# Optimization experiments

Measured on AMD Instinct MI355X. Metric: run time of the kernel, lower is better.

## Reference

```python
import jax, jax.numpy as jnp
import numpy as np

N_ITER = 3
N_CLASS = 10
N_ROUTE = 1152  # 32*6*6

def _conv(x, w, b, stride):
    y = jax.lax.conv_general_dilated(x, w, window_strides=(stride, stride), padding='VALID',
                                     dimension_numbers=('NCHW', 'OIHW', 'NCHW'))
    return y + b[None, :, None, None]

def setup_inputs() -> dict:
    key = jax.random.key(0)
    ks = jax.random.split(key, 7)
    B = 256
    return {
        'x': jax.random.normal(ks[0], (B, 1, 28, 28), jnp.float32),
        'conv1_w': jax.random.normal(ks[1], (256, 1, 9, 9), jnp.float32) * 0.05,
        'conv1_b': jax.random.normal(ks[2], (256,), jnp.float32) * 0.05,
        'conv2_w': jax.random.normal(ks[3], (256, 256, 9, 9), jnp.float32) * 0.02,
        'conv2_b': jax.random.normal(ks[4], (256,), jnp.float32) * 0.02,
        'W': jax.random.normal(ks[5], (10, 32, 6, 6, 16, 8), jnp.float32) * 0.1,
        'Wb': jax.random.normal(ks[6], (10, 32, 6, 6, 16), jnp.float32) * 0.1,
    }

def reference(x, conv1_w, conv1_b, conv2_w, conv2_b, W, Wb):
    # conv1 (no activation, matching the original forward)
    h = _conv(x, conv1_w, conv1_b, 1)                 # [B,256,20,20]
    prim = _conv(h, conv2_w, conv2_b, 2)              # [B,256,6,6]
    prim = prim.reshape(-1, 32, 6, 6, 8)              # same raw .view as torch
    # fused per-location linear: u_hat[b,j,k,l,i,o]
    u_hat = jnp.einsum('bjklc,ijkloc->bjklio', prim, W) + Wb.transpose(1, 2, 3, 0, 4)[None]
    B = u_hat.shape[0]
    xr = u_hat.reshape(B, N_CLASS, N_ROUTE, 16)       # same raw .view as torch
    bij = jnp.zeros((N_CLASS, N_ROUTE), u_hat.dtype)
    v = None
    for r in range(N_ITER):
        c = jax.nn.softmax(bij, axis=1)               # [10,1152]
        v = jnp.einsum('in,bink->bik', c, xr)         # [B,10,16]
        # squash over the whole [B,16] tensor per class i (as in original x.norm())
        nrm = jnp.sqrt(jnp.sum(v * v, axis=(0, 2), keepdims=True))
        n2 = nrm * nrm
        v = (n2 / (1.0 + n2)) * (v / nrm)
        if r < N_ITER - 1:
            bij = bij + jnp.einsum('bink,bik->in', xr, v)
    # torch.stack(outputs) -> [10,B,16], then .view(-1,10,16)
    return jnp.transpose(v, (1, 0, 2)).reshape(-1, N_CLASS, 16)
```

## Files before the change

kernel.cpp:

```cpp
#include <hip/hip_runtime.h>
#include <hip/hip_bf16.h>

#define DI __device__ __forceinline__

typedef unsigned int u32;
typedef unsigned short u16;
typedef __attribute__((ext_vector_type(8))) short short8;
typedef __attribute__((ext_vector_type(4))) float f32x4;

DI u16 f2bf(float f) {
  union { float f; u32 x; } t; t.f = f;
  u32 x = t.x;
  u32 r = (x + 0x7fffu + ((x >> 16) & 1u)) >> 16;
  return (u16)r;
}

typedef __attribute__((address_space(3))) u32 lds_u32;
typedef const __attribute__((address_space(1))) u32 gbl_u32;
DI void gl_lds16(const u16* g, u16* l) {
  __builtin_amdgcn_global_load_lds((gbl_u32*)(const void*)g, (lds_u32*)(void*)l, 16, 0, 0);
}

__global__ __launch_bounds__(256) void pre_kernel(
    const float* __restrict__ x, const float* __restrict__ w1,
    const float* __restrict__ b1, const float* __restrict__ w2,
    u16* __restrict__ hT, u16* __restrict__ w2bT) {
  __shared__ union {
    struct { u16 xbf[784]; u16 im[400 * 96]; u16 ws[256 * 96]; } c1;
    float w2s[5184];
  } S;
  int tid = threadIdx.x;
  if (blockIdx.x >= 256) {
    int oc = blockIdx.x - 256;
    for (int ch = 0; ch < 4; ++ch) {
      __syncthreads();
      for (int t = tid; t < 5184; t += 256) S.w2s[t] = w2[(size_t)oc * 20736 + ch * 5184 + t];
      __syncthreads();
      for (int t = tid; t < 5184; t += 256) {
        int tap = t >> 6, icl = t & 63;
        w2bT[((size_t)tap * 256 + oc) * 256 + ch * 64 + icl] = f2bf(S.w2s[icl * 81 + tap]);
      }
    }
    return;
  }
  int b = blockIdx.x;
  int lane = tid & 63, wid = tid >> 6;
  const float* xb = x + (size_t)b * 784;
  for (int t = tid; t < 784; t += 256) S.c1.xbf[t] = f2bf(xb[t]);
  for (int t = tid; t < 20736; t += 256) {
    int oc = t / 81, kk = t % 81;
    int g = (kk >> 3) & 3, ph = (kk & 96) | (((g ^ ((oc >> 1) & 3)) << 3)) | (kk & 7);
    S.c1.ws[oc * 96 + ph] = f2bf(w1[t]);
  }
  for (int t = tid; t < 256 * 15; t += 256) {
    int oc = t / 15, kk = 81 + t % 15;
    int g = (kk >> 3) & 3, ph = (kk & 96) | (((g ^ ((oc >> 1) & 3)) << 3)) | (kk & 7);
    S.c1.ws[oc * 96 + ph] = 0;
  }
  __syncthreads();
  for (int pix = tid; pix < 400; pix += 256) {
    int py = pix / 20, px = pix - py * 20;
    int c2 = (pix >> 1) & 3;
    u16* dst = &S.c1.im[pix * 96];
    const u16* src = &S.c1.xbf[py * 28 + px];
#pragma unroll
    for (int ky = 0; ky < 9; ++ky)
#pragma unroll
      for (int kx = 0; kx < 9; ++kx) {
        int kk = ky * 9 + kx;
        int ph = (kk & 96) | ((((kk >> 3) & 3) ^ c2) << 3) | (kk & 7);
        dst[ph] = src[ky * 28 + kx];
      }
#pragma unroll
    for (int kk = 81; kk < 96; ++kk) {
      int ph = (kk & 96) | ((((kk >> 3) & 3) ^ c2) << 3) | (kk & 7);
      dst[ph] = 0;
    }
  }
  __syncthreads();
  int l15 = lane & 15, lh = lane >> 4;
  int slot8 = (lh ^ ((l15 >> 1) & 3)) << 3;
  short8 br[4][3];
  float bias[4];
#pragma unroll
  for (int ni = 0; ni < 4; ++ni) {
    int row = wid * 64 + ni * 16 + l15;
    bias[ni] = b1[row];
#pragma unroll
    for (int ksb = 0; ksb < 3; ++ksb)
      br[ni][ksb] = *(const short8*)&S.c1.ws[row * 96 + ksb * 32 + slot8];
  }
  for (int mt = 0; mt < 25; ++mt) {
    f32x4 acc[4];
#pragma unroll
    for (int ni = 0; ni < 4; ++ni) acc[ni] = (f32x4){0.f, 0.f, 0.f, 0.f};
    short8 ar[3];
#pragma unroll
    for (int ksb = 0; ksb < 3; ++ksb)
      ar[ksb] = *(const short8*)&S.c1.im[(mt * 16 + l15) * 96 + ksb * 32 + slot8];
#pragma unroll
    for (int ksb = 0; ksb < 3; ++ksb)
#pragma unroll
      for (int ni = 0; ni < 4; ++ni)
        acc[ni] = __builtin_amdgcn_mfma_f32_16x16x32_bf16(ar[ksb], br[ni][ksb], acc[ni], 0, 0, 0);
#pragma unroll
    for (int ni = 0; ni < 4; ++ni)
#pragma unroll
      for (int reg = 0; reg < 4; ++reg)
        hT[((size_t)b * 400 + mt * 16 + lh * 4 + reg) * 256 + wid * 64 + ni * 16 + l15] =
            f2bf(acc[ni][reg] + bias[ni]);
  }
}

__global__ __launch_bounds__(512, 2) void conv2_mfma_kernel(
    const u16* __restrict__ hT, const u16* __restrict__ w2bT,
    float* __restrict__ pp) {
  __shared__ u16 Ab[3 * 8192];
  __shared__ u16 Bb[3 * 8192];
  int bid = blockIdx.x;
  int xcd = bid & 7, rank = bid >> 3;
  int work = (xcd < 4 ? xcd * 32 : 128 + (xcd - 4) * 31) + rank;
  int ks = work / 36, p = work % 36;
  int py = p / 6, px = p % 6;
  int tid = threadIdx.x, wid = tid >> 6, lane = tid & 63;
  int ntap = (ks < 4) ? 12 : 11;
  int nch = ntap * 8;

  int gsw = ((tid & 3) ^ ((tid >> 3) & 3)) * 8;
  int srow = tid >> 2;
  const u16* baseA0 = hT + (size_t)srow * 102400 + gsw;
  const u16* baseA1 = hT + (size_t)(128 + srow) * 102400 + gsw;
  const u16* baseB0 = w2bT + (size_t)srow * 256 + gsw;
  const u16* baseB1 = w2bT + (size_t)(128 + srow) * 256 + gsw;

#define STAGE(T, BUF) do {                                          \
    int tap_ = ((T) >> 3) * 7 + ks;                                 \
    int icc_ = ((T) & 7) << 5;                                      \
    int pix_ = (2 * py + tap_ / 9) * 20 + (2 * px + tap_ % 9);      \
    int tofsA_ = pix_ * 256 + icc_;                                 \
    size_t tofsB_ = (size_t)tap_ * 65536 + icc_;                    \
    u16* la_ = &Ab[(BUF) * 8192 + tid * 8];                         \
    u16* lb_ = &Bb[(BUF) * 8192 + tid * 8];                         \
    gl_lds16(baseA0 + tofsA_, la_);                                 \
    gl_lds16(baseA1 + tofsA_, la_ + 4096);                          \
    gl_lds16(baseB0 + tofsB_, lb_);                                 \
    gl_lds16(baseB1 + tofsB_, lb_ + 4096);                          \
  } while (0)

  f32x4 acc[8][4];
#pragma unroll
  for (int i = 0; i < 8; ++i)
#pragma unroll
    for (int j = 0; j < 4; ++j) acc[i][j] = (f32x4){0.f, 0.f, 0.f, 0.f};

  int wr = wid >> 2, wc = wid & 3;
  int l15 = lane & 15, lh = lane >> 4;

  STAGE(0, 0);
  STAGE(1, 1);

  int bufR = 0;
  for (int t = 0; t < nch; ++t) {
    if (t + 2 < nch) {
      int bufS = (bufR == 0) ? 2 : bufR - 1;
      STAGE(t + 2, bufS);
      asm volatile("s_waitcnt vmcnt(8)" ::: "memory");
    } else if (t + 1 < nch) {
      asm volatile("s_waitcnt vmcnt(4)" ::: "memory");
    } else {
      asm volatile("s_waitcnt vmcnt(0)" ::: "memory");
    }
    asm volatile("s_barrier" ::: "memory");
    const u16* A = &Ab[bufR * 8192];
    const u16* B = &Bb[bufR * 8192];
    short8 ar[8], br[4];
#pragma unroll
    for (int ni = 0; ni < 4; ++ni) {
      int row = wc * 64 + ni * 16 + l15;
      br[ni] = *(const short8*)&B[row * 32 + ((lh ^ ((row >> 1) & 3)) * 8)];
    }
#pragma unroll
    for (int mi = 0; mi < 8; ++mi) {
      int row = wr * 128 + mi * 16 + l15;
      ar[mi] = *(const short8*)&A[row * 32 + ((lh ^ ((row >> 1) & 3)) * 8)];
    }
    __builtin_amdgcn_s_setprio(1);
#pragma unroll
    for (int mi = 0; mi < 8; ++mi)
#pragma unroll
      for (int ni = 0; ni < 4; ++ni)
        acc[mi][ni] = __builtin_amdgcn_mfma_f32_16x16x32_bf16(ar[mi], br[ni], acc[mi][ni], 0, 0, 0);
    __builtin_amdgcn_s_setprio(0);
    asm volatile("s_barrier" ::: "memory");
    bufR = (bufR == 2) ? 0 : bufR + 1;
  }
#undef STAGE

  float* ppk = pp + (size_t)ks * 2359296 + (size_t)p * 256;
#pragma unroll
  for (int mi = 0; mi < 8; ++mi) {
    int b = wr * 128 + mi * 16 + lh * 4;
#pragma unroll
    for (int ni = 0; ni < 4; ++ni) {
      int oc = wc * 64 + ni * 16 + l15;
      *(float4*)&ppk[(size_t)oc * 9216 + b] = *(float4*)&acc[mi][ni];
    }
  }
}

__global__ __launch_bounds__(256) void cwvgemm_kernel(
    const float* __restrict__ bij, const float* __restrict__ W,
    const float* __restrict__ Wb, const float* __restrict__ pp,
    const float* __restrict__ b2, float* __restrict__ prim2T,
    float* __restrict__ vp, float* __restrict__ cbp, int first) {
  __shared__ float cS[1152];
  __shared__ float cws[512];
  __shared__ float red[256];
  __shared__ float cbl[40][16];
  int ch = blockIdx.x, i = blockIdx.y, tid = threadIdx.x;
  if (first) {
    for (int n = tid; n < 1152; n += 256) cS[n] = 1.0f / 1152.0f;
  } else {
    const float* brow = bij + i * 1152;
    float m = -1e30f;
    for (int n = tid; n < 1152; n += 256) m = fmaxf(m, brow[n]);
    red[tid] = m; __syncthreads();
    for (int s = 128; s > 0; s >>= 1) { if (tid < s) red[tid] = fmaxf(red[tid], red[tid + s]); __syncthreads(); }
    m = red[0]; __syncthreads();
    float sum = 0.f;
    for (int n = tid; n < 1152; n += 256) sum += expf(brow[n] - m);
    red[tid] = sum; __syncthreads();
    for (int s = 128; s > 0; s >>= 1) { if (tid < s) red[tid] += red[tid + s]; __syncthreads(); }
    float inv = 1.0f / red[0];
    for (int n = tid; n < 1152; n += 256) cS[n] = expf(brow[n] - m) * inv;
  }
  __syncthreads();
  int loc_min = (i * 1152) / 10, loc_max = ((i + 1) * 1152 - 1) / 10;
  int lc0 = loc_min + ch * 4;
  for (int t = tid; t < 512; t += 256) {
    int ll = t >> 7, rem = t & 127, k = rem >> 3, cc = rem & 7;
    int loc = lc0 + ll;
    float a = 0.f;
    if (loc <= loc_max) {
      for (int io = 0; io < 10; ++io) {
        int mm = loc * 10 + io;
        if (mm / 1152 == i)
          a += cS[mm - i * 1152] * W[(size_t)io * 147456 + (size_t)loc * 128 + k * 8 + cc];
      }
    }
    cws[ll * 128 + cc * 16 + k] = a;
  }
  if (tid < 40) {
    int ll = tid / 10, io = tid % 10;
    int loc = lc0 + ll;
    float cv = 0.f;
    if (loc <= loc_max) {
      int mm = loc * 10 + io;
      if (mm / 1152 == i) cv = cS[mm - i * 1152];
    }
    if (cv != 0.f) {
      const float* wb = Wb + (size_t)io * 18432 + (size_t)loc * 16;
#pragma unroll
      for (int k = 0; k < 16; ++k) cbl[tid][k] = cv * wb[k];
    } else {
#pragma unroll
      for (int k = 0; k < 16; ++k) cbl[tid][k] = 0.f;
    }
  }
  __syncthreads();
  if (tid < 16) {
    float s = 0.f;
    for (int q = 0; q < 40; ++q) s += cbl[q][tid];
    cbp[(size_t)(ch * 10 + i) * 16 + tid] = s;
  }
  float acc[16];
#pragma unroll
  for (int k = 0; k < 16; ++k) acc[k] = 0.f;
  for (int ll = 0; ll < 4; ++ll) {
    int loc = lc0 + ll;
    if (loc > loc_max) break;
    const float* cw = cws + ll * 128;
#pragma unroll
    for (int cc = 0; cc < 8; ++cc) {
      int flat = loc * 8 + cc;
      float pvv;
      if (first) {
        pvv = b2[flat / 36];
#pragma unroll
        for (int ks = 0; ks < 7; ++ks)
          pvv += pp[(size_t)ks * 2359296 + (size_t)flat * 256 + tid];
        prim2T[(size_t)flat * 256 + tid] = pvv;
      } else {
        pvv = prim2T[(size_t)flat * 256 + tid];
      }
      float4 a0 = *(const float4*)&cw[cc * 16];
      float4 a1 = *(const float4*)&cw[cc * 16 + 4];
      float4 a2 = *(const float4*)&cw[cc * 16 + 8];
      float4 a3 = *(const float4*)&cw[cc * 16 + 12];
      acc[0] += pvv * a0.x; acc[1] += pvv * a0.y; acc[2] += pvv * a0.z; acc[3] += pvv * a0.w;
      acc[4] += pvv * a1.x; acc[5] += pvv * a1.y; acc[6] += pvv * a1.z; acc[7] += pvv * a1.w;
      acc[8] += pvv * a2.x; acc[9] += pvv * a2.y; acc[10] += pvv * a2.z; acc[11] += pvv * a2.w;
      acc[12] += pvv * a3.x; acc[13] += pvv * a3.y; acc[14] += pvv * a3.z; acc[15] += pvv * a3.w;
    }
  }
  float* dst = vp + ((size_t)(ch * 10 + i) * 256 + tid) * 16;
#pragma unroll
  for (int k = 0; k < 16; ++k) dst[k] = acc[k];
}

__global__ __launch_bounds__(256) void vred_kernel(
    const float* __restrict__ vp, const float* __restrict__ cbp,
    float* __restrict__ vpre, float* __restrict__ ssp, float* __restrict__ svp) {
  __shared__ float red[256];
  __shared__ float sh[16][17];
  int bs = blockIdx.x, i = blockIdx.y, tid = threadIdx.x;
  int bl = tid >> 4, k = tid & 15;
  int b = bs * 16 + bl;
  float a = 0.f;
  for (int ch = 0; ch < 32; ++ch) a += vp[((size_t)(ch * 10 + i) * 256 + b) * 16 + k];
  float cb = 0.f;
  for (int ch = 0; ch < 32; ++ch) cb += cbp[(size_t)(ch * 10 + i) * 16 + k];
  a += cb;
  vpre[((size_t)i * 256 + b) * 16 + k] = a;
  red[tid] = a * a;
  sh[bl][k] = a;
  __syncthreads();
  for (int s = 128; s > 0; s >>= 1) { if (tid < s) red[tid] += red[tid + s]; __syncthreads(); }
  for (int s = 8; s > 0; s >>= 1) { if (bl < s) sh[bl][k] += sh[bl + s][k]; __syncthreads(); }
  if (tid == 0) ssp[i * 16 + bs] = red[0];
  if (tid < 16) svp[(size_t)(i * 16 + bs) * 16 + tid] = sh[0][tid];
}

__global__ __launch_bounds__(256) void pv_bij_kernel(
    const float* __restrict__ vpre, const float* __restrict__ ssp,
    const float* __restrict__ svp, const float* __restrict__ prim2T,
    const float* __restrict__ W, const float* __restrict__ Wb,
    float* __restrict__ bij, int first) {
  __shared__ float ps[32 * 260];
  __shared__ float vs[2 * 16 * 260];
  __shared__ float Ps[32][32];
  __shared__ float scl[2];
  __shared__ float svl[2][16];
  int blk = blockIdx.x, tid = threadIdx.x;
  int loc0 = blk * 4;
  int I = (loc0 * 10) / 1152;
  if (tid < 2) {
    int cls = I + tid;
    float ss = 0.f;
    if (cls <= 9)
      for (int q = 0; q < 16; ++q) ss += ssp[cls * 16 + q];
    float nrm = sqrtf(ss);
    scl[tid] = (cls <= 9 && nrm > 0.f) ? nrm / (1.f + nrm * nrm) : 0.f;
  }
  if (tid < 32) {
    int cl = tid >> 4, k = tid & 15;
    int cls = I + cl;
    float s = 0.f;
    if (cls <= 9)
      for (int q = 0; q < 16; ++q) s += svp[(size_t)(cls * 16 + q) * 16 + k];
    svl[cl][k] = s;
  }
  for (int t = tid; t < 2048; t += 256) {
    int row = t >> 6, seg = t & 63;
    float4 a = *(const float4*)(prim2T + (size_t)(loc0 * 8 + row) * 256 + seg * 4);
    *(float4*)&ps[row * 260 + seg * 4] = a;
  }
  __syncthreads();
  for (int cl = 0; cl < 2; ++cl) {
    int cls = I + cl;
    float sc = scl[cl];
    for (int t = tid; t < 4096; t += 256) {
      int b = t >> 4, k = t & 15;
      float val = (cls <= 9) ? vpre[(size_t)cls * 4096 + t] * sc : 0.f;
      vs[(cl * 16 + k) * 260 + b] = val;
    }
  }
  __syncthreads();
  {
    int k = tid & 15, fs = tid >> 4;
    const float4* ps4 = (const float4*)ps;
    const float4* vs4 = (const float4*)vs;
#pragma unroll
    for (int q = 0; q < 4; ++q) {
      int flat_l = fs * 2 + (q & 1);
      int slot = q >> 1;
      int loc = loc0 + (flat_l >> 3);
      int cls = (loc * 10) / 1152 + slot;
      int cl_idx = cls - I;
      if (cl_idx <= 1 && cls <= 9) {
        float a = 0.f;
        int bp = flat_l * 65, bv = (cl_idx * 16 + k) * 65;
        for (int b4 = 0; b4 < 64; ++b4) {
          float4 p4 = ps4[bp + b4];
          float4 w4 = vs4[bv + b4];
          a += p4.x * w4.x + p4.y * w4.y + p4.z * w4.z + p4.w * w4.w;
        }
        Ps[flat_l][slot * 16 + k] = a;
      }
    }
  }
  __syncthreads();
  if (tid < 40) {
    int ll = tid / 10, io = tid % 10;
    int loc = loc0 + ll;
    int m = loc * 10 + io;
    int i = m / 1152;
    int slot = i - (loc * 10) / 1152;
    int cl = i - I;
    const float* wrow = W + (size_t)io * 147456 + (size_t)loc * 128;
    float s = 0.f;
#pragma unroll
    for (int k = 0; k < 16; ++k) {
      float4 w0 = *(const float4*)(wrow + k * 8);
      float4 w1 = *(const float4*)(wrow + k * 8 + 4);
      s += w0.x * Ps[ll * 8 + 0][slot * 16 + k] + w0.y * Ps[ll * 8 + 1][slot * 16 + k]
         + w0.z * Ps[ll * 8 + 2][slot * 16 + k] + w0.w * Ps[ll * 8 + 3][slot * 16 + k];
      s += w1.x * Ps[ll * 8 + 4][slot * 16 + k] + w1.y * Ps[ll * 8 + 5][slot * 16 + k]
         + w1.z * Ps[ll * 8 + 6][slot * 16 + k] + w1.w * Ps[ll * 8 + 7][slot * 16 + k];
    }
    const float* wbr = Wb + (size_t)io * 18432 + (size_t)loc * 16;
    float scsv = scl[cl];
#pragma unroll
    for (int k = 0; k < 16; ++k) s += wbr[k] * (scsv * svl[cl][k]);
    bij[m] = first ? s : (bij[m] + s);
  }
}

__global__ __launch_bounds__(256) void outw_kernel(
    const float* __restrict__ vpre, const float* __restrict__ ssp,
    float* __restrict__ out) {
  int i = blockIdx.x, tid = threadIdx.x;
  float ss = 0.f;
  for (int q = 0; q < 16; ++q) ss += ssp[i * 16 + q];
  float nrm = sqrtf(ss);
  float scale = (nrm > 0.f) ? nrm / (1.f + nrm * nrm) : 0.f;
  for (int t = tid; t < 4096; t += 256)
    out[(size_t)i * 4096 + t] = vpre[(size_t)i * 4096 + t] * scale;
}

extern "C" void kernel_launch(void* const* d_in, const int* in_sizes, int n_in,
                              void* d_out, int out_size, void* d_ws, size_t ws_size,
                              hipStream_t stream) {
  const float* x  = (const float*)d_in[0];
  const float* w1 = (const float*)d_in[1];
  const float* b1 = (const float*)d_in[2];
  const float* w2 = (const float*)d_in[3];
  const float* b2 = (const float*)d_in[4];
  const float* W  = (const float*)d_in[5];
  const float* Wb = (const float*)d_in[6];
  float* out = (float*)d_out;

  u16*   hT     = (u16*)d_ws;
  u16*   w2bT   = hT + 26214400;
  float* pp     = (float*)(w2bT + 5308416);
  float* prim2T = pp + 7 * 2359296;
  float* vp     = prim2T + 2359296;
  float* vpre   = vp + 1310720;
  float* bij    = vpre + 40960;
  float* ssp    = bij + 11520;
  float* svp    = ssp + 160;
  float* cbp    = svp + 2560;

  pre_kernel<<<512, 256, 0, stream>>>(x, w1, b1, w2, hT, w2bT);
  conv2_mfma_kernel<<<252, 512, 0, stream>>>(hT, w2bT, pp);

  for (int r = 0; r < 3; ++r) {
    cwvgemm_kernel<<<dim3(32, 10), 256, 0, stream>>>(bij, W, Wb, pp, b2, prim2T, vp, cbp,
                                                     r == 0 ? 1 : 0);
    vred_kernel<<<dim3(16, 10), 256, 0, stream>>>(vp, cbp, vpre, ssp, svp);
    if (r < 2) {
      pv_bij_kernel<<<288, 256, 0, stream>>>(vpre, ssp, svp, prim2T, W, Wb, bij,
                                             r == 0 ? 1 : 0);
    } else {
      outw_kernel<<<10, 256, 0, stream>>>(vpre, ssp, out);
    }
  }
}
```

Measured before the change: 308.0 us.

## Load conv2 weights directly to registers and double K-chunk width per stage

Restructures the conv2 MFMA main loop so that only the activation tile goes through LDS, now staged in 64-wide K chunks via a triple buffer with a new swizzle. The weight fragments are loaded straight from global memory into registers and double-buffered one chunk ahead. Each chunk now covers twice the K depth, which halves the number of loop iterations and barriers. The aim is to cut LDS traffic and synchronisation overhead in exchange for more registers and uncoalesced-per-wave global weight loads, with implicit compiler waitcnts replacing the explicit vmcnt pipelining.

```diff
diff --git a/kernel.cpp b/kernel.cpp
--- a/kernel.cpp
+++ b/kernel.cpp
@@ -115,8 +115,7 @@
 __global__ __launch_bounds__(512, 2) void conv2_mfma_kernel(
     const u16* __restrict__ hT, const u16* __restrict__ w2bT,
     float* __restrict__ pp) {
-  __shared__ u16 Ab[3 * 8192];
-  __shared__ u16 Bb[3 * 8192];
+  __shared__ u16 Ab[3][16384];
   int bid = blockIdx.x;
   int xcd = bid & 7, rank = bid >> 3;
   int work = (xcd < 4 ? xcd * 32 : 128 + (xcd - 4) * 31) + rank;
@@ -124,77 +123,81 @@
   int py = p / 6, px = p % 6;
   int tid = threadIdx.x, wid = tid >> 6, lane = tid & 63;
   int ntap = (ks < 4) ? 12 : 11;
-  int nch = ntap * 8;
-
-  int gsw = ((tid & 3) ^ ((tid >> 3) & 3)) * 8;
-  int srow = tid >> 2;
-  const u16* baseA0 = hT + (size_t)srow * 102400 + gsw;
-  const u16* baseA1 = hT + (size_t)(128 + srow) * 102400 + gsw;
-  const u16* baseB0 = w2bT + (size_t)srow * 256 + gsw;
-  const u16* baseB1 = w2bT + (size_t)(128 + srow) * 256 + gsw;
-
-#define STAGE(T, BUF) do {                                          \
-    int tap_ = ((T) >> 3) * 7 + ks;                                 \
-    int icc_ = ((T) & 7) << 5;                                      \
-    int pix_ = (2 * py + tap_ / 9) * 20 + (2 * px + tap_ % 9);      \
-    int tofsA_ = pix_ * 256 + icc_;                                 \
-    size_t tofsB_ = (size_t)tap_ * 65536 + icc_;                    \
-    u16* la_ = &Ab[(BUF) * 8192 + tid * 8];                         \
-    u16* lb_ = &Bb[(BUF) * 8192 + tid * 8];                         \
-    gl_lds16(baseA0 + tofsA_, la_);                                 \
-    gl_lds16(baseA1 + tofsA_, la_ + 4096);                          \
-    gl_lds16(baseB0 + tofsB_, lb_);                                 \
-    gl_lds16(baseB1 + tofsB_, lb_ + 4096);                          \
-  } while (0)
-
-  f32x4 acc[8][4];
-#pragma unroll
-  for (int i = 0; i < 8; ++i)
-#pragma unroll
-    for (int j = 0; j < 4; ++j) acc[i][j] = (f32x4){0.f, 0.f, 0.f, 0.f};
+  int nch = ntap * 4;
+
+  const u16* srcA[4];
+#pragma unroll
+  for (int c = 0; c < 4; ++c) {
+    int row = wid * 32 + c * 8 + (lane >> 3);
+    int gsw = ((lane & 7) ^ (row & 7)) * 8;
+    srcA[c] = hT + (size_t)row * 102400 + gsw;
+  }
 
   int wr = wid >> 2, wc = wid & 3;
   int l15 = lane & 15, lh = lane >> 4;
-
-  STAGE(0, 0);
-  STAGE(1, 1);
-
-  int bufR = 0;
-  for (int t = 0; t < nch; ++t) {
-    if (t + 2 < nch) {
-      int bufS = (bufR == 0) ? 2 : bufR - 1;
-      STAGE(t + 2, bufS);
-      asm volatile("s_waitcnt vmcnt(8)" ::: "memory");
-    } else if (t + 1 < nch) {
-      asm volatile("s_waitcnt vmcnt(4)" ::: "memory");
-    } else {
-      asm volatile("s_waitcnt vmcnt(0)" ::: "memory");
-    }
-    asm volatile("s_barrier" ::: "memory");
-    const u16* A = &Ab[bufR * 8192];
-    const u16* B = &Bb[bufR * 8192];
-    short8 ar[8], br[4];
-#pragma unroll
-    for (int ni = 0; ni < 4; ++ni) {
-      int row = wc * 64 + ni * 16 + l15;
-      br[ni] = *(const short8*)&B[row * 32 + ((lh ^ ((row >> 1) & 3)) * 8)];
-    }
-#pragma unroll
-    for (int mi = 0; mi < 8; ++mi) {
-      int row = wr * 128 + mi * 16 + l15;
-      ar[mi] = *(const short8*)&A[row * 32 + ((lh ^ ((row >> 1) & 3)) * 8)];
-    }
-    __builtin_amdgcn_s_setprio(1);
-#pragma unroll
-    for (int mi = 0; mi < 8; ++mi)
-#pragma unroll
-      for (int ni = 0; ni < 4; ++ni)
-        acc[mi][ni] = __builtin_amdgcn_mfma_f32_16x16x32_bf16(ar[mi], br[ni], acc[mi][ni], 0, 0, 0);
-    __builtin_amdgcn_s_setprio(0);
-    asm volatile("s_barrier" ::: "memory");
+  const u16* pB[4];
+#pragma unroll
+  for (int ni = 0; ni < 4; ++ni)
+    pB[ni] = w2bT + (size_t)(wc * 64 + ni * 16 + l15) * 256 + lh * 8;
+
+  f32x4 acc[8][4];
+#pragma unroll
+  for (int i = 0; i < 8; ++i)
+#pragma unroll
+    for (int j = 0; j < 4; ++j) acc[i][j] = (f32x4){0.f, 0.f, 0.f, 0.f};
+
+#define STAGEA(T, BUF) do {                                          \
+    int tap_ = ((T) >> 2) * 7 + ks;                                  \
+    int icc_ = ((T) & 3) << 6;                                       \
+    int pix_ = (2 * py + tap_ / 9) * 20 + (2 * px + tap_ % 9);       \
+    int tofs_ = pix_ * 256 + icc_;                                   \
+    _Pragma("unroll")                                                \
+    for (int c_ = 0; c_ < 4; ++c_)                                   \
+      gl_lds16(srcA[c_] + tofs_, &Ab[BUF][(wid * 32 + c_ * 8) * 64]);\
+  } while (0)
+
+#define LOADB(T, DST) do {                                           \
+    int tap_ = ((T) >> 2) * 7 + ks;                                  \
+    size_t off_ = (size_t)tap_ * 65536 + (size_t)(((T) & 3) << 6);   \
+    _Pragma("unroll")                                                \
+    for (int ni_ = 0; ni_ < 4; ++ni_) {                              \
+      DST[0][ni_] = *(const short8*)(pB[ni_] + off_);                \
+      DST[1][ni_] = *(const short8*)(pB[ni_] + off_ + 32);           \
+    }                                                                \
+  } while (0)
+
+  short8 brc[2][4], brn[2][4];
+  STAGEA(0, 0);
+  STAGEA(1, 1);
+  LOADB(0, brc);
+
+  int bufR = 0, bufS = 2;
+  for (int ch = 0; ch < nch; ++ch) {
+    __syncthreads();
+    if (ch + 2 < nch) STAGEA(ch + 2, bufS);
+    if (ch + 1 < nch) LOADB(ch + 1, brn);
+    const u16* A = &Ab[bufR][0];
+#pragma unroll
+    for (int kk = 0; kk < 2; ++kk) {
+      int g = kk * 4 + lh;
+#pragma unroll
+      for (int mi = 0; mi < 8; ++mi) {
+        int row = wr * 128 + mi * 16 + l15;
+        short8 ar = *(const short8*)&A[row * 64 + ((g ^ (row & 7)) * 8)];
+#pragma unroll
+        for (int ni = 0; ni < 4; ++ni)
+          acc[mi][ni] = __builtin_amdgcn_mfma_f32_16x16x32_bf16(ar, brc[kk][ni], acc[mi][ni], 0, 0, 0);
+      }
+    }
+#pragma unroll
+    for (int kk = 0; kk < 2; ++kk)
+#pragma unroll
+      for (int ni = 0; ni < 4; ++ni) brc[kk][ni] = brn[kk][ni];
     bufR = (bufR == 2) ? 0 : bufR + 1;
-  }
-#undef STAGE
+    bufS = (bufS == 2) ? 0 : bufS + 1;
+  }
+#undef STAGEA
+#undef LOADB
 
   float* ppk = pp + (size_t)ks * 2359296 + (size_t)p * 256;
 #pragma unroll
```

New measurement: 339.2 us. +10.2%, slower.

## Double split-K in conv2 to 14 slices with bf16 partials and double buffering

Applied to the files above, without the earlier changes.

Conv2 split-K goes from 7 to 14 tap groups, so 504 blocks launch instead of 252, and launch bounds are raised to 4 blocks per CU. The LDS pipeline shrinks from triple to double buffering with plain __syncthreads, and the setprio hints are dropped. Partial sums are stored as bf16 instead of fp32 to halve the extra partial traffic, then summed in fp32 by the consumer. The aim is better CU occupancy and parallelism, at the cost of more partial-sum reads, extra rounding error from bf16 partials, and less latency hiding in the load pipeline.

```diff
diff --git a/kernel.cpp b/kernel.cpp
--- a/kernel.cpp
+++ b/kernel.cpp
@@ -14,6 +14,7 @@
   u32 r = (x + 0x7fffu + ((x >> 16) & 1u)) >> 16;
   return (u16)r;
 }
+DI float bfu(u16 v) { union { u32 x; float f; } t; t.x = ((u32)v) << 16; return t.f; }
 
 typedef __attribute__((address_space(3))) u32 lds_u32;
 typedef const __attribute__((address_space(1))) u32 gbl_u32;
@@ -112,18 +113,18 @@
   }
 }
 
-__global__ __launch_bounds__(512, 2) void conv2_mfma_kernel(
+__global__ __launch_bounds__(512, 4) void conv2_mfma_kernel(
     const u16* __restrict__ hT, const u16* __restrict__ w2bT,
-    float* __restrict__ pp) {
-  __shared__ u16 Ab[3 * 8192];
-  __shared__ u16 Bb[3 * 8192];
+    u16* __restrict__ pp) {
+  __shared__ u16 Ab[2][8192];
+  __shared__ u16 Bb[2][8192];
   int bid = blockIdx.x;
   int xcd = bid & 7, rank = bid >> 3;
-  int work = (xcd < 4 ? xcd * 32 : 128 + (xcd - 4) * 31) + rank;
+  int work = xcd * 63 + rank;
   int ks = work / 36, p = work % 36;
   int py = p / 6, px = p % 6;
   int tid = threadIdx.x, wid = tid >> 6, lane = tid & 63;
-  int ntap = (ks < 4) ? 12 : 11;
+  int ntap = (ks < 11) ? 6 : 5;
   int nch = ntap * 8;
 
   int gsw = ((tid & 3) ^ ((tid >> 3) & 3)) * 8;
@@ -134,13 +135,13 @@
   const u16* baseB1 = w2bT + (size_t)(128 + srow) * 256 + gsw;
 
 #define STAGE(T, BUF) do {                                          \
-    int tap_ = ((T) >> 3) * 7 + ks;                                 \
+    int tap_ = ((T) >> 3) * 14 + ks;                                \
     int icc_ = ((T) & 7) << 5;                                      \
     int pix_ = (2 * py + tap_ / 9) * 20 + (2 * px + tap_ % 9);      \
     int tofsA_ = pix_ * 256 + icc_;                                 \
     size_t tofsB_ = (size_t)tap_ * 65536 + icc_;                    \
-    u16* la_ = &Ab[(BUF) * 8192 + tid * 8];                         \
-    u16* lb_ = &Bb[(BUF) * 8192 + tid * 8];                         \
+    u16* la_ = &Ab[BUF][tid * 8];                                   \
+    u16* lb_ = &Bb[BUF][tid * 8];                                   \
     gl_lds16(baseA0 + tofsA_, la_);                                 \
     gl_lds16(baseA1 + tofsA_, la_ + 4096);                          \
     gl_lds16(baseB0 + tofsB_, lb_);                                 \
@@ -157,23 +158,14 @@
   int l15 = lane & 15, lh = lane >> 4;
 
   STAGE(0, 0);
-  STAGE(1, 1);
-
-  int bufR = 0;
-  for (int t = 0; t < nch; ++t) {
-    if (t + 2 < nch) {
-      int bufS = (bufR == 0) ? 2 : bufR - 1;
-      STAGE(t + 2, bufS);
-      asm volatile("s_waitcnt vmcnt(8)" ::: "memory");
-    } else if (t + 1 < nch) {
-      asm volatile("s_waitcnt vmcnt(4)" ::: "memory");
-    } else {
-      asm volatile("s_waitcnt vmcnt(0)" ::: "memory");
-    }
-    asm volatile("s_barrier" ::: "memory");
-    const u16* A = &Ab[bufR * 8192];
-    const u16* B = &Bb[bufR * 8192];
-    short8 ar[8], br[4];
+
+  for (int ch = 0; ch < nch; ++ch) {
+    __syncthreads();
+    int buf = ch & 1;
+    if (ch + 1 < nch) STAGE(ch + 1, buf ^ 1);
+    const u16* A = &Ab[buf][0];
+    const u16* B = &Bb[buf][0];
+    short8 br[4];
 #pragma unroll
     for (int ni = 0; ni < 4; ++ni) {
       int row = wc * 64 + ni * 16 + l15;
@@ -182,35 +174,32 @@
 #pragma unroll
     for (int mi = 0; mi < 8; ++mi) {
       int row = wr * 128 + mi * 16 + l15;
-      ar[mi] = *(const short8*)&A[row * 32 + ((lh ^ ((row >> 1) & 3)) * 8)];
-    }
-    __builtin_amdgcn_s_setprio(1);
-#pragma unroll
-    for (int mi = 0; mi < 8; ++mi)
+      short8 ar = *(const short8*)&A[row * 32 + ((lh ^ ((row >> 1) & 3)) * 8)];
 #pragma unroll
       for (int ni = 0; ni < 4; ++ni)
-        acc[mi][ni] = __builtin_amdgcn_mfma_f32_16x16x32_bf16(ar[mi], br[ni], acc[mi][ni], 0, 0, 0);
-    __builtin_amdgcn_s_setprio(0);
-    asm volatile("s_barrier" ::: "memory");
-    bufR = (bufR == 2) ? 0 : bufR + 1;
+        acc[mi][ni] = __builtin_amdgcn_mfma_f32_16x16x32_bf16(ar, br[ni], acc[mi][ni], 0, 0, 0);
+    }
   }
 #undef STAGE
 
-  float* ppk = pp + (size_t)ks * 2359296 + (size_t)p * 256;
+  u16* ppk = pp + (size_t)ks * 2359296 + (size_t)p * 256;
 #pragma unroll
   for (int mi = 0; mi < 8; ++mi) {
     int b = wr * 128 + mi * 16 + lh * 4;
 #pragma unroll
     for (int ni = 0; ni < 4; ++ni) {
       int oc = wc * 64 + ni * 16 + l15;
-      *(float4*)&ppk[(size_t)oc * 9216 + b] = *(float4*)&acc[mi][ni];
+      union { u16 h[4]; uint2 u; } pk;
+#pragma unroll
+      for (int reg = 0; reg < 4; ++reg) pk.h[reg] = f2bf(acc[mi][ni][reg]);
+      *(uint2*)&ppk[(size_t)oc * 9216 + b] = pk.u;
     }
   }
 }
 
 __global__ __launch_bounds__(256) void cwvgemm_kernel(
     const float* __restrict__ bij, const float* __restrict__ W,
-    const float* __restrict__ Wb, const float* __restrict__ pp,
+    const float* __restrict__ Wb, const u16* __restrict__ pp,
     const float* __restrict__ b2, float* __restrict__ prim2T,
     float* __restrict__ vp, float* __restrict__ cbp, int first) {
   __shared__ float cS[1152];
@@ -287,8 +276,8 @@
       if (first) {
         pvv = b2[flat / 36];
 #pragma unroll
-        for (int ks = 0; ks < 7; ++ks)
-          pvv += pp[(size_t)ks * 2359296 + (size_t)flat * 256 + tid];
+        for (int ks = 0; ks < 14; ++ks)
+          pvv += bfu(pp[(size_t)ks * 2359296 + (size_t)flat * 256 + tid]);
         prim2T[(size_t)flat * 256 + tid] = pvv;
       } else {
         pvv = prim2T[(size_t)flat * 256 + tid];
@@ -452,8 +441,8 @@
 
   u16*   hT     = (u16*)d_ws;
   u16*   w2bT   = hT + 26214400;
-  float* pp     = (float*)(w2bT + 5308416);
-  float* prim2T = pp + 7 * 2359296;
+  u16*   pp     = w2bT + 5308416;
+  float* prim2T = (float*)(pp + 14 * 2359296);
   float* vp     = prim2T + 2359296;
   float* vpre   = vp + 1310720;
   float* bij    = vpre + 40960;
@@ -462,7 +451,7 @@
   float* cbp    = svp + 2560;
 
   pre_kernel<<<512, 256, 0, stream>>>(x, w1, b1, w2, hT, w2bT);
-  conv2_mfma_kernel<<<252, 512, 0, stream>>>(hT, w2bT, pp);
+  conv2_mfma_kernel<<<504, 512, 0, stream>>>(hT, w2bT, pp);
 
   for (int r = 0; r < 3; ++r) {
     cwvgemm_kernel<<<dim3(32, 10), 256, 0, stream>>>(bij, W, Wb, pp, b2, prim2T, vp, cbp,
```

New measurement: 807.1 us. 2.62x slower.
